# Optimization experiments

Hardware: AMD Instinct MI355X
Metric: run time of the kernel (lower is better)

## Reference

```python
import jax, jax.numpy as jnp
import numpy as np

B = 8            # number of point clouds in the batch
NT = 8192        # target points per cloud
NS = 2048        # source points per cloud
K = 3            # knn_interpolate neighbors
C_TGT = 128      # target (skip) feature channels
C_SRC = 256      # source feature channels
C_IN = C_TGT + C_SRC   # 384 = mlp_channels[0]
C_HID = 256            # mlp_channels[1]
C_OUT = 128            # mlp_channels[2]
EPS = 1e-16


def setup_inputs() -> dict:
    key = jax.random.key(0)
    ks = jax.random.split(key, 10)
    Nt, Ns = B * NT, B * NS
    s1 = 1.0 / np.sqrt(C_IN)
    s2 = 1.0 / np.sqrt(C_HID)
    return {
        "x_target": jax.random.normal(ks[0], (Nt, C_TGT), jnp.float32),
        "pos_target": jax.random.normal(ks[1], (Nt, 3), jnp.float32),
        "batch_target": (jnp.arange(Nt, dtype=jnp.int32) // NT).astype(jnp.int32),
        "x_source": jax.random.normal(ks[2], (Ns, C_SRC), jnp.float32),
        "pos_source": jax.random.normal(ks[3], (Ns, 3), jnp.float32),
        "batch_source": (jnp.arange(Ns, dtype=jnp.int32) // NS).astype(jnp.int32),
        "W1": jax.random.normal(ks[4], (C_IN, C_HID), jnp.float32) * s1,
        "b1": jnp.zeros((C_HID,), jnp.float32),
        "W2": jax.random.normal(ks[5], (C_HID, C_OUT), jnp.float32) * s2,
        "b2": jnp.zeros((C_OUT,), jnp.float32),
        "Ws": jax.random.normal(ks[6], (C_IN, C_OUT), jnp.float32) * s1,
        "bs": jnp.zeros((C_OUT,), jnp.float32),
    }


def _knn_interpolate(x_source, pos_source, pos_target):
    """PyG knn_interpolate with inverse-squared-distance weights.
    Batches are contiguous equal-size blocks -> reshape to [B, N, ...]."""
    pt = pos_target.reshape(B, NT, 3)
    ps = pos_source.reshape(B, NS, 3)
    xs = x_source.reshape(B, NS, C_SRC)
    # squared pairwise distances [B, NT, NS]
    d2 = jnp.sum((pt[:, :, None, :] - ps[:, None, :, :]) ** 2, axis=-1)
    neg, idx = jax.lax.top_k(-d2, K)            # idx: [B, NT, K]
    w = 1.0 / jnp.clip(-neg, EPS)               # inverse squared distance
    gathered = jax.vmap(lambda x, i: x[i])(xs, idx)  # [B, NT, K, C_SRC]
    interp = jnp.sum(w[..., None] * gathered, axis=2) / jnp.sum(w, axis=2)[..., None]
    return interp.reshape(B * NT, C_SRC)


def reference(x_target, pos_target, batch_target, x_source, pos_source,
              batch_source, W1, b1, W2, b2, Ws, bs):
    interpolated = _knn_interpolate(x_source, pos_source, pos_target)
    combined = jnp.concatenate([x_target, interpolated], axis=1)  # [Nt, 384]
    h = jax.nn.relu(combined @ W1 + b1) @ W2 + b2                 # MLP branch
    res = combined @ Ws + bs                                      # shortcut
    return jax.nn.relu(h + res)
```

## Files before the change

kernel.cpp:

```cpp
#include <hip/hip_runtime.h>
#include <hip/hip_bf16.h>

#define B_    8
#define NT_   8192
#define NS_   2048
#define NTOT  (B_ * NT_)
#define CTGT  128
#define CSRC  256
#define CIN   384
#define CHID  256
#define COUT  128

typedef __bf16 bf16x8 __attribute__((ext_vector_type(8)));
typedef float  f32x4  __attribute__((ext_vector_type(4)));
typedef unsigned short u16x8 __attribute__((ext_vector_type(8)));

__device__ inline unsigned short f2bf(float f) {
    unsigned int u = __float_as_uint(f);
    u += 0x7FFF + ((u >> 16) & 1);
    return (unsigned short)(u >> 16);
}

__global__ __launch_bounds__(256) void prep_weights(
    const float* __restrict__ W1, const float* __restrict__ Ws,
    const float* __restrict__ W2,
    unsigned short* __restrict__ Wct, unsigned short* __restrict__ W2t) {
    int g = blockIdx.x * 256 + threadIdx.x;
    if (g < CIN * CIN) {
        int n = g / CIN, k = g % CIN;
        float v = (n < CHID) ? W1[(size_t)k * CHID + n]
                             : Ws[(size_t)k * COUT + (n - CHID)];
        Wct[g] = f2bf(v);
    } else {
        int g2 = g - CIN * CIN;
        if (g2 < COUT * CHID) {
            int n = g2 / CHID, k = g2 % CHID;
            W2t[g2] = f2bf(W2[(size_t)k * COUT + n]);
        }
    }
}

__global__ __launch_bounds__(256) void knn_kernel(
    const float* __restrict__ pos_t, const float* __restrict__ pos_s,
    int* __restrict__ knn_i, float* __restrict__ knn_d) {
    __shared__ float4 ps4[NS_];
    __shared__ float  md[256 * 3];
    __shared__ int    mi[256 * 3];

    int blk = blockIdx.x;
    int batch = blk >> 8;
    const float* src = pos_s + (size_t)batch * NS_ * 3;
    for (int i = threadIdx.x; i < NS_; i += 256) {
        ps4[i] = make_float4(src[i * 3 + 0], src[i * 3 + 1], src[i * 3 + 2], 0.0f);
    }
    __syncthreads();

    int tl = threadIdx.x & 31;
    int ck = threadIdx.x >> 5;
    int t = blk * 32 + tl;
    float ptx = pos_t[t * 3 + 0];
    float pty = pos_t[t * 3 + 1];
    float ptz = pos_t[t * 3 + 2];

    float d0 = 3.4e38f, d1 = 3.4e38f, d2v = 3.4e38f;
    int i0 = 0, i1 = 0, i2 = 0;
    int jbeg = ck * 256, jend = jbeg + 256;
#pragma unroll 4
    for (int j = jbeg; j < jend; ++j) {
        float4 p = ps4[j];
        float dx = __fsub_rn(ptx, p.x);
        float dy = __fsub_rn(pty, p.y);
        float dz = __fsub_rn(ptz, p.z);
        float d = __fadd_rn(__fadd_rn(__fmul_rn(dx, dx), __fmul_rn(dy, dy)),
                            __fmul_rn(dz, dz));
        if (d < d2v) {
            if (d < d1) {
                d2v = d1; i2 = i1;
                if (d < d0) { d1 = d0; i1 = i0; d0 = d; i0 = j; }
                else        { d1 = d;  i1 = j; }
            } else { d2v = d; i2 = j; }
        }
    }
    int slot = (tl * 8 + ck) * 3;
    md[slot + 0] = d0;  md[slot + 1] = d1;  md[slot + 2] = d2v;
    mi[slot + 0] = i0;  mi[slot + 1] = i1;  mi[slot + 2] = i2;
    __syncthreads();

    if (ck == 0) {
        float e0 = md[tl * 24 + 0], e1 = md[tl * 24 + 1], e2 = md[tl * 24 + 2];
        int   j0 = mi[tl * 24 + 0], j1 = mi[tl * 24 + 1], j2 = mi[tl * 24 + 2];
#pragma unroll
        for (int c = 1; c < 8; ++c) {
#pragma unroll
            for (int r = 0; r < 3; ++r) {
                float d = md[tl * 24 + c * 3 + r];
                int   i = mi[tl * 24 + c * 3 + r];
                if (d < e2) {
                    if (d < e1) {
                        e2 = e1; j2 = j1;
                        if (d < e0) { e1 = e0; j1 = j0; e0 = d; j0 = i; }
                        else        { e1 = d;  j1 = i; }
                    } else { e2 = d; j2 = i; }
                }
            }
        }
        knn_i[t * 3 + 0] = j0; knn_i[t * 3 + 1] = j1; knn_i[t * 3 + 2] = j2;
        knn_d[t * 3 + 0] = e0; knn_d[t * 3 + 1] = e1; knn_d[t * 3 + 2] = e2;
    }
}

__global__ __launch_bounds__(256) void interp_kernel(
    const float* __restrict__ x_t, const float* __restrict__ x_s,
    const int* __restrict__ knn_i, const float* __restrict__ knn_d,
    unsigned short* __restrict__ combined) {
    int g = blockIdx.x * 256 + threadIdx.x;
    int row = g / 96, seg = g % 96;
    if (row >= NTOT) return;
    if (seg < 32) {
        float4 v = *(const float4*)(x_t + (size_t)row * CTGT + seg * 4);
        ushort4 o;
        o.x = f2bf(v.x); o.y = f2bf(v.y); o.z = f2bf(v.z); o.w = f2bf(v.w);
        *(ushort4*)(combined + (size_t)row * CIN + seg * 4) = o;
    } else {
        int c = (seg - 32) * 4;
        int batch = row >> 13;
        const float* xsb = x_s + (size_t)batch * NS_ * CSRC;
        int i0 = knn_i[row * 3 + 0];
        int i1 = knn_i[row * 3 + 1];
        int i2 = knn_i[row * 3 + 2];
        float w0 = 1.0f / fmaxf(knn_d[row * 3 + 0], 1e-16f);
        float w1 = 1.0f / fmaxf(knn_d[row * 3 + 1], 1e-16f);
        float w2 = 1.0f / fmaxf(knn_d[row * 3 + 2], 1e-16f);
        float inv = 1.0f / (w0 + w1 + w2);
        float4 a = *(const float4*)(xsb + (size_t)i0 * CSRC + c);
        float4 b = *(const float4*)(xsb + (size_t)i1 * CSRC + c);
        float4 d = *(const float4*)(xsb + (size_t)i2 * CSRC + c);
        ushort4 o;
        o.x = f2bf((w0 * a.x + w1 * b.x + w2 * d.x) * inv);
        o.y = f2bf((w0 * a.y + w1 * b.y + w2 * d.y) * inv);
        o.z = f2bf((w0 * a.z + w1 * b.z + w2 * d.z) * inv);
        o.w = f2bf((w0 * a.w + w1 * b.w + w2 * d.w) * inv);
        *(ushort4*)(combined + (size_t)row * CIN + CTGT + c) = o;
    }
}

__global__ __launch_bounds__(256) void gemm1_kernel(
    const unsigned short* __restrict__ A, const unsigned short* __restrict__ Bt,
    const float* __restrict__ b1, const float* __restrict__ bs,
    unsigned short* __restrict__ hbuf, float* __restrict__ resbuf) {
    __shared__ unsigned short Alds[128 * 40];
    __shared__ unsigned short Blds[128 * 40];
    int bm = blockIdx.x;
    int bn = blockIdx.y;
    int tid = threadIdx.x;
    int wid = tid >> 6, lane = tid & 63;
    int wm = wid >> 1, wn = wid & 1;
    int lrow = lane & 15;
    int kgrp = (lane >> 4) * 8;

    f32x4 acc[4][4] = {};

    for (int k0 = 0; k0 < CIN; k0 += 32) {
#pragma unroll
        for (int i = 0; i < 2; ++i) {
            int c = tid + i * 256;
            int row = c >> 2, kk = (c & 3) * 8;
            u16x8 va = *(const u16x8*)(A + (size_t)(bm * 128 + row) * CIN + k0 + kk);
            *(u16x8*)(&Alds[row * 40 + kk]) = va;
            u16x8 vb = *(const u16x8*)(Bt + (size_t)(bn * 128 + row) * CIN + k0 + kk);
            *(u16x8*)(&Blds[row * 40 + kk]) = vb;
        }
        __syncthreads();
        bf16x8 af[4], bf[4];
#pragma unroll
        for (int mi = 0; mi < 4; ++mi)
            af[mi] = *(const bf16x8*)(&Alds[(wm * 64 + mi * 16 + lrow) * 40 + kgrp]);
#pragma unroll
        for (int ni = 0; ni < 4; ++ni)
            bf[ni] = *(const bf16x8*)(&Blds[(wn * 64 + ni * 16 + lrow) * 40 + kgrp]);
#pragma unroll
        for (int mi = 0; mi < 4; ++mi)
#pragma unroll
            for (int ni = 0; ni < 4; ++ni)
                acc[mi][ni] = __builtin_amdgcn_mfma_f32_16x16x32_bf16(
                    af[mi], bf[ni], acc[mi][ni], 0, 0, 0);
        __syncthreads();
    }

    int r0 = (lane >> 4) * 4;
#pragma unroll
    for (int mi = 0; mi < 4; ++mi)
#pragma unroll
        for (int ni = 0; ni < 4; ++ni) {
            int n = bn * 128 + wn * 64 + ni * 16 + lrow;
#pragma unroll
            for (int r = 0; r < 4; ++r) {
                int m = bm * 128 + wm * 64 + mi * 16 + r0 + r;
                float v = acc[mi][ni][r];
                if (n < CHID) {
                    v += b1[n];
                    v = fmaxf(v, 0.0f);
                    hbuf[(size_t)m * CHID + n] = f2bf(v);
                } else {
                    int n2 = n - CHID;
                    resbuf[(size_t)m * COUT + n2] = v + bs[n2];
                }
            }
        }
}

__global__ __launch_bounds__(256) void gemm2_kernel(
    const unsigned short* __restrict__ A, const unsigned short* __restrict__ Bt,
    const float* __restrict__ b2, const float* __restrict__ resbuf,
    float* __restrict__ out) {
    __shared__ unsigned short Alds[128 * 40];
    __shared__ unsigned short Blds[128 * 40];
    int bm = blockIdx.x;
    int tid = threadIdx.x;
    int wid = tid >> 6, lane = tid & 63;
    int wm = wid >> 1, wn = wid & 1;
    int lrow = lane & 15;
    int kgrp = (lane >> 4) * 8;

    f32x4 acc[4][4] = {};

    for (int k0 = 0; k0 < CHID; k0 += 32) {
#pragma unroll
        for (int i = 0; i < 2; ++i) {
            int c = tid + i * 256;
            int row = c >> 2, kk = (c & 3) * 8;
            u16x8 va = *(const u16x8*)(A + (size_t)(bm * 128 + row) * CHID + k0 + kk);
            *(u16x8*)(&Alds[row * 40 + kk]) = va;
            u16x8 vb = *(const u16x8*)(Bt + (size_t)row * CHID + k0 + kk);
            *(u16x8*)(&Blds[row * 40 + kk]) = vb;
        }
        __syncthreads();
        bf16x8 af[4], bf[4];
#pragma unroll
        for (int mi = 0; mi < 4; ++mi)
            af[mi] = *(const bf16x8*)(&Alds[(wm * 64 + mi * 16 + lrow) * 40 + kgrp]);
#pragma unroll
        for (int ni = 0; ni < 4; ++ni)
            bf[ni] = *(const bf16x8*)(&Blds[(wn * 64 + ni * 16 + lrow) * 40 + kgrp]);
#pragma unroll
        for (int mi = 0; mi < 4; ++mi)
#pragma unroll
            for (int ni = 0; ni < 4; ++ni)
                acc[mi][ni] = __builtin_amdgcn_mfma_f32_16x16x32_bf16(
                    af[mi], bf[ni], acc[mi][ni], 0, 0, 0);
        __syncthreads();
    }

    int r0 = (lane >> 4) * 4;
#pragma unroll
    for (int mi = 0; mi < 4; ++mi)
#pragma unroll
        for (int ni = 0; ni < 4; ++ni) {
            int n = wn * 64 + ni * 16 + lrow;
#pragma unroll
            for (int r = 0; r < 4; ++r) {
                int m = bm * 128 + wm * 64 + mi * 16 + r0 + r;
                float v = acc[mi][ni][r] + b2[n] + resbuf[(size_t)m * COUT + n];
                out[(size_t)m * COUT + n] = fmaxf(v, 0.0f);
            }
        }
}

extern "C" void kernel_launch(void* const* d_in, const int* in_sizes, int n_in,
                              void* d_out, int out_size, void* d_ws, size_t ws_size,
                              hipStream_t stream) {
    const float* x_t   = (const float*)d_in[0];
    const float* pos_t = (const float*)d_in[1];
    const float* x_s   = (const float*)d_in[3];
    const float* pos_s = (const float*)d_in[4];
    const float* W1    = (const float*)d_in[6];
    const float* b1    = (const float*)d_in[7];
    const float* W2    = (const float*)d_in[8];
    const float* b2    = (const float*)d_in[9];
    const float* Ws    = (const float*)d_in[10];
    const float* bs    = (const float*)d_in[11];

    char* ws = (char*)d_ws;
    int*            knn_i  = (int*)           (ws + 0);
    float*          knn_d  = (float*)         (ws + 786432);
    unsigned short* Wct    = (unsigned short*)(ws + 1572864);
    unsigned short* W2t    = (unsigned short*)(ws + 1867776);
    unsigned short* comb   = (unsigned short*)(ws + 1933312);
    unsigned short* hbuf   = (unsigned short*)(ws + 52264960);
    float*          resbuf = (float*)         (ws + 85819392);
    float*          out    = (float*)d_out;

    prep_weights<<<704, 256, 0, stream>>>(W1, Ws, W2, Wct, W2t);
    knn_kernel<<<NTOT / 32, 256, 0, stream>>>(pos_t, pos_s, knn_i, knn_d);
    interp_kernel<<<(NTOT * 96) / 256, 256, 0, stream>>>(x_t, x_s, knn_i, knn_d, comb);
    dim3 g1(NTOT / 128, CIN / 128);
    gemm1_kernel<<<g1, 256, 0, stream>>>(comb, Wct, b1, bs, hbuf, resbuf);
    gemm2_kernel<<<NTOT / 128, 256, 0, stream>>>(hbuf, W2t, b2, resbuf, out);
}
```

Measured before the change: 304.4 us.

## Double-buffer GEMM LDS tiles with direct global-to-LDS loads and XOR swizzle

```diff
diff --git a/kernel.cpp b/kernel.cpp
--- a/kernel.cpp
+++ b/kernel.cpp
@@ -19,6 +19,28 @@
     unsigned int u = __float_as_uint(f);
     u += 0x7FFF + ((u >> 16) & 1);
     return (unsigned short)(u >> 16);
+}
+
+__device__ __forceinline__ void gload16(const unsigned short* g, unsigned short* l) {
+    __builtin_amdgcn_global_load_lds(
+        (const __attribute__((address_space(1))) unsigned int*)g,
+        (__attribute__((address_space(3))) unsigned int*)l, 16, 0, 0);
+}
+
+__device__ __forceinline__ void stage_ab(
+    const unsigned short* __restrict__ ga, int ldA,
+    const unsigned short* __restrict__ gb, int ldB,
+    unsigned short* Alds, unsigned short* Blds,
+    int k0, int widu, int lane) {
+    int rloc = lane >> 2;
+    int cswz = ((lane & 3) ^ ((lane >> 3) & 3)) * 8;
+#pragma unroll
+    for (int i = 0; i < 2; ++i) {
+        int c = widu * 2 + i;
+        int row = c * 16 + rloc;
+        gload16(ga + (size_t)row * ldA + k0 + cswz, Alds + c * 512);
+        gload16(gb + (size_t)row * ldB + k0 + cswz, Blds + c * 512);
+    }
 }
 
 __global__ __launch_bounds__(256) void prep_weights(
@@ -148,36 +170,35 @@
     const unsigned short* __restrict__ A, const unsigned short* __restrict__ Bt,
     const float* __restrict__ b1, const float* __restrict__ bs,
     unsigned short* __restrict__ hbuf, float* __restrict__ resbuf) {
-    __shared__ unsigned short Alds[128 * 40];
-    __shared__ unsigned short Blds[128 * 40];
-    int bm = blockIdx.x;
-    int bn = blockIdx.y;
+    __shared__ unsigned short Alds[2][128 * 32];
+    __shared__ unsigned short Blds[2][128 * 32];
     int tid = threadIdx.x;
     int wid = tid >> 6, lane = tid & 63;
+    int widu = __builtin_amdgcn_readfirstlane(wid);
     int wm = wid >> 1, wn = wid & 1;
-    int lrow = lane & 15;
-    int kgrp = (lane >> 4) * 8;
+    int r = lane & 15, g = lane >> 4;
+    int kcol = (g * 8) ^ (((r >> 1) & 3) * 8);
+
+    const unsigned short* ga = A  + (size_t)(blockIdx.x * 128) * CIN;
+    const unsigned short* gb = Bt + (size_t)(blockIdx.y * 128) * CIN;
 
     f32x4 acc[4][4] = {};
 
-    for (int k0 = 0; k0 < CIN; k0 += 32) {
-#pragma unroll
-        for (int i = 0; i < 2; ++i) {
-            int c = tid + i * 256;
-            int row = c >> 2, kk = (c & 3) * 8;
-            u16x8 va = *(const u16x8*)(A + (size_t)(bm * 128 + row) * CIN + k0 + kk);
-            *(u16x8*)(&Alds[row * 40 + kk]) = va;
-            u16x8 vb = *(const u16x8*)(Bt + (size_t)(bn * 128 + row) * CIN + k0 + kk);
-            *(u16x8*)(&Blds[row * 40 + kk]) = vb;
-        }
-        __syncthreads();
+    stage_ab(ga, CIN, gb, CIN, Alds[0], Blds[0], 0, widu, lane);
+    __syncthreads();
+    int cur = 0;
+#pragma unroll 1
+    for (int t = 0; t < 12; ++t) {
+        if (t + 1 < 12)
+            stage_ab(ga, CIN, gb, CIN, Alds[cur ^ 1], Blds[cur ^ 1],
+                     (t + 1) * 32, widu, lane);
         bf16x8 af[4], bf[4];
 #pragma unroll
         for (int mi = 0; mi < 4; ++mi)
-            af[mi] = *(const bf16x8*)(&Alds[(wm * 64 + mi * 16 + lrow) * 40 + kgrp]);
+            af[mi] = *(const bf16x8*)(&Alds[cur][(wm * 64 + mi * 16 + r) * 32 + kcol]);
 #pragma unroll
         for (int ni = 0; ni < 4; ++ni)
-            bf[ni] = *(const bf16x8*)(&Blds[(wn * 64 + ni * 16 + lrow) * 40 + kgrp]);
+            bf[ni] = *(const bf16x8*)(&Blds[cur][(wn * 64 + ni * 16 + r) * 32 + kcol]);
 #pragma unroll
         for (int mi = 0; mi < 4; ++mi)
 #pragma unroll
@@ -185,18 +206,19 @@
                 acc[mi][ni] = __builtin_amdgcn_mfma_f32_16x16x32_bf16(
                     af[mi], bf[ni], acc[mi][ni], 0, 0, 0);
         __syncthreads();
-    }
-
-    int r0 = (lane >> 4) * 4;
+        cur ^= 1;
+    }
+
+    int r0 = g * 4;
 #pragma unroll
     for (int mi = 0; mi < 4; ++mi)
 #pragma unroll
         for (int ni = 0; ni < 4; ++ni) {
-            int n = bn * 128 + wn * 64 + ni * 16 + lrow;
-#pragma unroll
-            for (int r = 0; r < 4; ++r) {
-                int m = bm * 128 + wm * 64 + mi * 16 + r0 + r;
-                float v = acc[mi][ni][r];
+            int n = blockIdx.y * 128 + wn * 64 + ni * 16 + r;
+#pragma unroll
+            for (int rr = 0; rr < 4; ++rr) {
+                int m = blockIdx.x * 128 + wm * 64 + mi * 16 + r0 + rr;
+                float v = acc[mi][ni][rr];
                 if (n < CHID) {
                     v += b1[n];
                     v = fmaxf(v, 0.0f);
@@ -213,35 +235,34 @@
     const unsigned short* __restrict__ A, const unsigned short* __restrict__ Bt,
     const float* __restrict__ b2, const float* __restrict__ resbuf,
     float* __restrict__ out) {
-    __shared__ unsigned short Alds[128 * 40];
-    __shared__ unsigned short Blds[128 * 40];
-    int bm = blockIdx.x;
+    __shared__ unsigned short Alds[2][128 * 32];
+    __shared__ unsigned short Blds[2][128 * 32];
     int tid = threadIdx.x;
     int wid = tid >> 6, lane = tid & 63;
+    int widu = __builtin_amdgcn_readfirstlane(wid);
     int wm = wid >> 1, wn = wid & 1;
-    int lrow = lane & 15;
-    int kgrp = (lane >> 4) * 8;
+    int r = lane & 15, g = lane >> 4;
+    int kcol = (g * 8) ^ (((r >> 1) & 3) * 8);
+
+    const unsigned short* ga = A + (size_t)(blockIdx.x * 128) * CHID;
 
     f32x4 acc[4][4] = {};
 
-    for (int k0 = 0; k0 < CHID; k0 += 32) {
-#pragma unroll
-        for (int i = 0; i < 2; ++i) {
-            int c = tid + i * 256;
-            int row = c >> 2, kk = (c & 3) * 8;
-            u16x8 va = *(const u16x8*)(A + (size_t)(bm * 128 + row) * CHID + k0 + kk);
-            *(u16x8*)(&Alds[row * 40 + kk]) = va;
-            u16x8 vb = *(const u16x8*)(Bt + (size_t)row * CHID + k0 + kk);
-            *(u16x8*)(&Blds[row * 40 + kk]) = vb;
-        }
-        __syncthreads();
+    stage_ab(ga, CHID, Bt, CHID, Alds[0], Blds[0], 0, widu, lane);
+    __syncthreads();
+    int cur = 0;
+#pragma unroll 1
+    for (int t = 0; t < 8; ++t) {
+        if (t + 1 < 8)
+            stage_ab(ga, CHID, Bt, CHID, Alds[cur ^ 1], Blds[cur ^ 1],
+                     (t + 1) * 32, widu, lane);
         bf16x8 af[4], bf[4];
 #pragma unroll
         for (int mi = 0; mi < 4; ++mi)
-            af[mi] = *(const bf16x8*)(&Alds[(wm * 64 + mi * 16 + lrow) * 40 + kgrp]);
+            af[mi] = *(const bf16x8*)(&Alds[cur][(wm * 64 + mi * 16 + r) * 32 + kcol]);
 #pragma unroll
         for (int ni = 0; ni < 4; ++ni)
-            bf[ni] = *(const bf16x8*)(&Blds[(wn * 64 + ni * 16 + lrow) * 40 + kgrp]);
+            bf[ni] = *(const bf16x8*)(&Blds[cur][(wn * 64 + ni * 16 + r) * 32 + kcol]);
 #pragma unroll
         for (int mi = 0; mi < 4; ++mi)
 #pragma unroll
@@ -249,18 +270,19 @@
                 acc[mi][ni] = __builtin_amdgcn_mfma_f32_16x16x32_bf16(
                     af[mi], bf[ni], acc[mi][ni], 0, 0, 0);
         __syncthreads();
-    }
-
-    int r0 = (lane >> 4) * 4;
+        cur ^= 1;
+    }
+
+    int r0 = g * 4;
 #pragma unroll
     for (int mi = 0; mi < 4; ++mi)
 #pragma unroll
         for (int ni = 0; ni < 4; ++ni) {
-            int n = wn * 64 + ni * 16 + lrow;
-#pragma unroll
-            for (int r = 0; r < 4; ++r) {
-                int m = bm * 128 + wm * 64 + mi * 16 + r0 + r;
-                float v = acc[mi][ni][r] + b2[n] + resbuf[(size_t)m * COUT + n];
+            int n = wn * 64 + ni * 16 + r;
+#pragma unroll
+            for (int rr = 0; rr < 4; ++rr) {
+                int m = blockIdx.x * 128 + wm * 64 + mi * 16 + r0 + rr;
+                float v = acc[mi][ni][rr] + b2[n] + resbuf[(size_t)m * COUT + n];
                 out[(size_t)m * COUT + n] = fmaxf(v, 0.0f);
             }
         }
```

Result: faster. 275.0 us (-9.7%).
